# Kernel tuning notes

Measured on AMD Instinct MI355X. Metric: run time of the kernel, lower is better.

## Reference

```python
import jax, jax.numpy as jnp
import numpy as np

N_NODES = 25000
N_EDGES = 400000
FEAT = 128
HID = 64
HEADS = 4
NUM_CLASSES = 2
NUM_GRAPHS = 64


def setup_inputs() -> dict:
    key = jax.random.key(0)
    ks = jax.random.split(key, 16)
    x = jax.random.normal(ks[0], (N_NODES, FEAT), dtype=jnp.float32)
    edge_index = jax.random.randint(ks[1], (2, N_EDGES), 0, N_NODES, dtype=jnp.int32)
    batch = jnp.sort(jax.random.randint(ks[2], (N_NODES,), 0, NUM_GRAPHS, dtype=jnp.int32))
    s = 1.0 / np.sqrt(FEAT)
    sh = 1.0 / np.sqrt(HID)
    shc = 1.0 / np.sqrt(HID * HEADS)
    return {
        "x": x,
        "edge_index": edge_index,
        "batch": batch,
        # conv1: GraphConv(FEAT -> HID): lin_rel (bias) on aggregated neighbors + lin_root (no bias)
        "W1_rel": jax.random.uniform(ks[3], (FEAT, HID), jnp.float32, -s, s),
        "b1": jnp.zeros((HID,), jnp.float32),
        "W1_root": jax.random.uniform(ks[4], (FEAT, HID), jnp.float32, -s, s),
        # conv3: GATConv(HID -> HID, heads=HEADS), concat output [N, HEADS*HID]
        "Wg": jax.random.uniform(ks[5], (HID, HEADS * HID), jnp.float32, -sh, sh),
        "att_src": jax.random.uniform(ks[6], (HEADS, HID), jnp.float32, -sh, sh),
        "att_dst": jax.random.uniform(ks[7], (HEADS, HID), jnp.float32, -sh, sh),
        "bg": jnp.zeros((HEADS * HID,), jnp.float32),
        # conv5: GraphConv(HEADS*HID -> HID)
        "W5_rel": jax.random.uniform(ks[8], (HEADS * HID, HID), jnp.float32, -shc, shc),
        "b5": jnp.zeros((HID,), jnp.float32),
        "W5_root": jax.random.uniform(ks[9], (HEADS * HID, HID), jnp.float32, -shc, shc),
        # fc head
        "W_fc1": jax.random.uniform(ks[10], (HID, HID), jnp.float32, -sh, sh),
        "b_fc1": jnp.zeros((HID,), jnp.float32),
        "W_fc2": jax.random.uniform(ks[11], (HID, NUM_CLASSES), jnp.float32, -sh, sh),
        "b_fc2": jnp.zeros((NUM_CLASSES,), jnp.float32),
    }


def _graph_conv(h, src, dst, W_rel, b, W_root):
    # PyG GraphConv (aggr='add'): out_i = W_rel @ sum_{j->i} h_j + b + W_root @ h_i
    agg = jax.ops.segment_sum(h[src], dst, num_segments=N_NODES)
    return agg @ W_rel + b + h @ W_root


def _gat_conv(h, src, dst, Wg, att_src, att_dst, bg):
    # GATConv with default add_self_loops=True; eval mode (no attn dropout)
    n = h.shape[0]
    loop = jnp.arange(n, dtype=src.dtype)
    si = jnp.concatenate([src, loop])
    di = jnp.concatenate([dst, loop])
    xl = (h @ Wg).reshape(n, HEADS, HID)              # [N, H, C]
    a_s = jnp.sum(xl * att_src, axis=-1)              # [N, H]
    a_d = jnp.sum(xl * att_dst, axis=-1)              # [N, H]
    e = jax.nn.leaky_relu(a_s[si] + a_d[di], 0.2)     # [E', H]
    m = jax.ops.segment_max(e, di, num_segments=n)
    p = jnp.exp(e - m[di])
    denom = jax.ops.segment_sum(p, di, num_segments=n)
    alpha = p / denom[di]                             # segment softmax over incoming edges
    out = jax.ops.segment_sum(alpha[:, :, None] * xl[si], di, num_segments=n)
    return out.reshape(n, HEADS * HID) + bg


def reference(x, edge_index, batch, W1_rel, b1, W1_root, Wg, att_src, att_dst, bg,
              W5_rel, b5, W5_root, W_fc1, b_fc1, W_fc2, b_fc2):
    src, dst = edge_index[0], edge_index[1]
    h = jax.nn.relu(_graph_conv(x, src, dst, W1_rel, b1, W1_root))
    h = jax.nn.relu(_gat_conv(h, src, dst, Wg, att_src, att_dst, bg))
    h = jax.nn.relu(_graph_conv(h, src, dst, W5_rel, b5, W5_root))
    g = jax.ops.segment_sum(h, batch, num_segments=NUM_GRAPHS)   # global_add_pool
    g = jax.nn.relu(g @ W_fc1 + b_fc1)
    return jax.nn.sigmoid(g @ W_fc2 + b_fc2)
```

## Files before the change

kernel.cpp:

```cpp
#include <hip/hip_runtime.h>
#include <math.h>

#define N_NODES 25000
#define N_EDGES 400000
#define FEAT 128
#define HID 64
#define HEADS 4
#define HH 256
#define NUM_GRAPHS 64
#define BUCKET 96
#define HS 1601536
#define NPH 25600

typedef unsigned short ushort_t;
typedef unsigned int uint_t;
typedef __attribute__((ext_vector_type(8))) short short8;
typedef __attribute__((ext_vector_type(4))) float f32x4;

__device__ __forceinline__ float lrelu(float x){ return x > 0.f ? x : 0.2f*x; }

__device__ __forceinline__ ushort_t f2bf(float f){
  uint_t u = __float_as_uint(f);
  return (ushort_t)((u + 0x7fffu + ((u >> 16) & 1u)) >> 16);
}
#define BF_LO(u) __uint_as_float((u) << 16)
#define BF_HI(u) __uint_as_float((u) & 0xffff0000u)

__global__ __launch_bounds__(256) void k_fill(
    const int* __restrict__ src, const int* __restrict__ dst,
    int* __restrict__ cnt, int* __restrict__ slot,
    const float* __restrict__ W1_rel, const float* __restrict__ W1_root,
    const float* __restrict__ W5_rel, const float* __restrict__ W5_root,
    const float* __restrict__ Wg,
    ushort_t* __restrict__ wc1b, ushort_t* __restrict__ wc5b,
    ushort_t* __restrict__ wgb)
{
  const int e = blockIdx.x*256 + threadIdx.x;
  if (blockIdx.x < 64){
    {
      int j=e&7, lane=(e>>3)&63, kc=(e>>9)&3, nt=e>>11;
      int k = kc*32 + (lane>>4)*8 + j, n = nt*16 + (lane&15);
      float v = (n < 64) ? W1_rel[k*64 + n] : W1_root[k*64 + n - 64];
      wc1b[e] = f2bf(v);
    }
    {
      int j=e&7, lane=(e>>3)&63, kt=(e>>9)&1, nt=e>>10;
      int k = kt*32 + (lane>>4)*8 + j, n = nt*16 + (lane&15);
      wgb[e] = f2bf(Wg[k*HH + n]);
    }
    #pragma unroll
    for (int e5 = e; e5 < 32768; e5 += 16384){
      int j=e5&7, lane=(e5>>3)&63, kc=(e5>>9)&7, nt=e5>>12;
      int k = kc*32 + (lane>>4)*8 + j, n = nt*16 + (lane&15);
      float v = (n < 64) ? W5_rel[k*64 + n] : W5_root[k*64 + n - 64];
      wc5b[e5] = f2bf(v);
    }
  }
  if (e < N_EDGES){
    int d = dst[e];
    int pos = atomicAdd(&cnt[d], 1);
    if (pos < BUCKET) slot[(size_t)d*BUCKET + pos] = src[e];
  }
}

__global__ __launch_bounds__(256) void conv1_mfma(
    const float* __restrict__ X, const ushort_t* __restrict__ wc1b,
    const float* __restrict__ bias,
    ushort_t* __restrict__ out_rel_b, float* __restrict__ out_root)
{
  const int wid  = __builtin_amdgcn_readfirstlane(threadIdx.x >> 6);
  const int lane = threadIdx.x & 63;
  const int quad = lane >> 4, col = lane & 15;
  const int nb = blockIdx.x*64 + wid*16;
  if (nb >= N_NODES) return;
  const int row = min(nb + col, N_NODES-1);
  const float* __restrict__ xr = X + (size_t)row*FEAT + quad*8;
  short8 a[4];
  #pragma unroll
  for (int kc = 0; kc < 4; kc++){
    #pragma unroll
    for (int j = 0; j < 8; j++)
      ((ushort_t*)&a[kc])[j] = f2bf(xr[kc*32 + j]);
  }
  #pragma unroll
  for (int nt = 0; nt < 8; nt++){
    f32x4 d = {0.f,0.f,0.f,0.f};
    #pragma unroll
    for (int kc = 0; kc < 4; kc++){
      short8 b = *(const short8*)(wc1b + ((size_t)(nt*4+kc)*64 + lane)*8);
      d = __builtin_amdgcn_mfma_f32_16x16x32_bf16(a[kc], b, d, 0, 0, 0);
    }
    if (nt < 4){
      #pragma unroll
      for (int r = 0; r < 4; r++){
        const int node = nb + quad*4 + r;
        if (node < N_NODES)
          out_rel_b[(size_t)node*HID + nt*16 + col] = f2bf(d[r]);
      }
    } else {
      const float bv = bias[(nt-4)*16 + col];
      #pragma unroll
      for (int r = 0; r < 4; r++){
        const int node = nb + quad*4 + r;
        if (node < N_NODES)
          out_root[(size_t)node*HID + (nt-4)*16 + col] = d[r] + bv;
      }
    }
  }
}

__global__ __launch_bounds__(256) void conv5_mfma(
    const ushort_t* __restrict__ h2b_hm, const ushort_t* __restrict__ wc5b,
    const float* __restrict__ bias,
    ushort_t* __restrict__ out_rel_b, float* __restrict__ out_root)
{
  const int wid  = __builtin_amdgcn_readfirstlane(threadIdx.x >> 6);
  const int lane = threadIdx.x & 63;
  const int quad = lane >> 4, col = lane & 15;
  const int nb = blockIdx.x*64 + wid*16;
  if (nb >= N_NODES) return;
  const int row = nb + col;
  short8 a[8];
  #pragma unroll
  for (int kc = 0; kc < 8; kc++){
    const int k0 = kc*32 + quad*8;
    a[kc] = *(const short8*)(h2b_hm + (size_t)(k0>>6)*HS
                             + (size_t)row*HID + (k0&63));
  }
  #pragma unroll
  for (int nt = 0; nt < 8; nt++){
    f32x4 d = {0.f,0.f,0.f,0.f};
    #pragma unroll
    for (int kc = 0; kc < 8; kc++){
      short8 b = *(const short8*)(wc5b + ((size_t)(nt*8+kc)*64 + lane)*8);
      d = __builtin_amdgcn_mfma_f32_16x16x32_bf16(a[kc], b, d, 0, 0, 0);
    }
    if (nt < 4){
      #pragma unroll
      for (int r = 0; r < 4; r++){
        const int node = nb + quad*4 + r;
        if (node < N_NODES)
          out_rel_b[(size_t)node*HID + nt*16 + col] = f2bf(d[r]);
      }
    } else {
      const float bv = bias[(nt-4)*16 + col];
      #pragma unroll
      for (int r = 0; r < 4; r++){
        const int node = nb + quad*4 + r;
        if (node < N_NODES)
          out_root[(size_t)node*HID + (nt-4)*16 + col] = d[r] + bv;
      }
    }
  }
}

__global__ __launch_bounds__(256) void k3_mfma(
    const ushort_t* __restrict__ h1b, const ushort_t* __restrict__ wgb,
    const float* __restrict__ att_src, const float* __restrict__ att_dst,
    ushort_t* __restrict__ xlb_hm, float* __restrict__ a_s_hm,
    float* __restrict__ a_d_hm)
{
  const int wid  = __builtin_amdgcn_readfirstlane(threadIdx.x >> 6);
  const int lane = threadIdx.x & 63;
  const int quad = lane >> 4, col = lane & 15;
  const int nb = blockIdx.x*64 + wid*16;
  const ushort_t* arow = h1b + (size_t)(nb + col)*HID + quad*8;
  short8 a0 = *(const short8*)(arow);
  short8 a1 = *(const short8*)(arow + 32);
  float as_acc[4] = {0,0,0,0}, ad_acc[4] = {0,0,0,0};
  #pragma unroll
  for (int nt = 0; nt < 16; nt++){
    short8 b0 = *(const short8*)(wgb + ((size_t)(nt*2+0)*64 + lane)*8);
    short8 b1 = *(const short8*)(wgb + ((size_t)(nt*2+1)*64 + lane)*8);
    f32x4 d = {0.f, 0.f, 0.f, 0.f};
    d = __builtin_amdgcn_mfma_f32_16x16x32_bf16(a0, b0, d, 0, 0, 0);
    d = __builtin_amdgcn_mfma_f32_16x16x32_bf16(a1, b1, d, 0, 0, 0);
    const int h = nt >> 2;
    const float asv = att_src[h*HID + (nt & 3)*16 + col];
    const float adv = att_dst[h*HID + (nt & 3)*16 + col];
    #pragma unroll
    for (int r = 0; r < 4; r++){
      const int node = nb + quad*4 + r;
      if (node < N_NODES)
        xlb_hm[(size_t)h*HS + (size_t)node*HID + (nt&3)*16 + col] = f2bf(d[r]);
      as_acc[r] += d[r]*asv;
      ad_acc[r] += d[r]*adv;
    }
    if ((nt & 3) == 3){
      #pragma unroll
      for (int r = 0; r < 4; r++){
        float s1 = as_acc[r], s2 = ad_acc[r];
        #pragma unroll
        for (int off = 1; off < 16; off <<= 1){
          s1 += __shfl_xor(s1, off, 64);
          s2 += __shfl_xor(s2, off, 64);
        }
        const int node = nb + quad*4 + r;
        if (col == 0 && node < N_NODES){
          a_s_hm[h*NPH + node] = s1;
          a_d_hm[h*NPH + node] = s2;
        }
        as_acc[r] = 0.f; ad_acc[r] = 0.f;
      }
    }
  }
}

template<bool BF16OUT>
__global__ __launch_bounds__(256) void k_aggb(
    const int* __restrict__ cnt, const int* __restrict__ slot,
    const ushort_t* __restrict__ featb, const float* __restrict__ root,
    float* __restrict__ outf, ushort_t* __restrict__ outb)
{
  const int node = blockIdx.x*4 + (threadIdx.x >> 6);
  const int lane = threadIdx.x & 63;
  const int* __restrict__ sl = slot + (size_t)node*BUCKET;
  const int deg = min(cnt[node], BUCKET);
  float acc = root[(size_t)node*HID + lane];
  int e = 0;
  for (; e + 4 <= deg; e += 4){
    int sA = sl[e],   sB = sl[e+1];
    int sC = sl[e+2], sD = sl[e+3];
    float xA = BF_LO((uint_t)featb[(size_t)sA*HID + lane]);
    float xB = BF_LO((uint_t)featb[(size_t)sB*HID + lane]);
    float xC = BF_LO((uint_t)featb[(size_t)sC*HID + lane]);
    float xD = BF_LO((uint_t)featb[(size_t)sD*HID + lane]);
    acc += xA; acc += xB; acc += xC; acc += xD;
  }
  for (; e < deg; e++){
    int s = sl[e];
    acc += BF_LO((uint_t)featb[(size_t)s*HID + lane]);
  }
  const float v = fmaxf(acc, 0.f);
  if (BF16OUT) outb[(size_t)node*HID + lane] = f2bf(v);
  else         outf[(size_t)node*HID + lane] = v;
}

__global__ __launch_bounds__(256) void k_gat_node(
    const int* __restrict__ cnt, const int* __restrict__ slot,
    const ushort_t* __restrict__ xlb_hm, const float* __restrict__ a_s_hm,
    const float* __restrict__ a_d_hm, const float* __restrict__ bg,
    ushort_t* __restrict__ h2b_hm)
{
  const int head = blockIdx.x & 3;
  const int node = (blockIdx.x >> 2)*16 + (threadIdx.x >> 4);
  if (node >= N_NODES) return;
  const int lane = threadIdx.x & 63;
  const int cl = lane & 15;
  const int gb = lane & 48;
  const int* __restrict__ sl = slot + (size_t)node*BUCKET;
  const int deg = min(cnt[node], BUCKET);
  const ushort_t* __restrict__ xlh = xlb_hm + (size_t)head*HS;
  const float* __restrict__ ash = a_s_hm + head*NPH;
  const float adh = a_d_hm[head*NPH + node];
  float acc0=0, acc1=0, acc2=0, acc3=0;
  float dsum = 0.f;
  for (int base = 0; base < deg; base += 16){
    float pme = 0.f; int sme = node;
    const int e = base + cl;
    if (e < deg){
      sme = sl[e];
      pme = __expf(lrelu(ash[sme] + adh));
    }
    dsum += pme;
    const int nsub = min(16, deg - base);
    int s = 0;
    for (; s + 2 <= nsub; s += 2){
      const float pA = __shfl(pme, gb + s, 64);
      const int   sA = __shfl(sme, gb + s, 64);
      const float pB = __shfl(pme, gb + s + 1, 64);
      const int   sB = __shfl(sme, gb + s + 1, 64);
      uint2 rA = ((const uint2*)(xlh + (size_t)sA*HID))[cl];
      uint2 rB = ((const uint2*)(xlh + (size_t)sB*HID))[cl];
      acc0 += pA*BF_LO(rA.x); acc1 += pA*BF_HI(rA.x);
      acc2 += pA*BF_LO(rA.y); acc3 += pA*BF_HI(rA.y);
      acc0 += pB*BF_LO(rB.x); acc1 += pB*BF_HI(rB.x);
      acc2 += pB*BF_LO(rB.y); acc3 += pB*BF_HI(rB.y);
    }
    if (s < nsub){
      const float pA = __shfl(pme, gb + s, 64);
      const int   sA = __shfl(sme, gb + s, 64);
      uint2 rA = ((const uint2*)(xlh + (size_t)sA*HID))[cl];
      acc0 += pA*BF_LO(rA.x); acc1 += pA*BF_HI(rA.x);
      acc2 += pA*BF_LO(rA.y); acc3 += pA*BF_HI(rA.y);
    }
  }
  #pragma unroll
  for (int off = 1; off < 16; off <<= 1) dsum += __shfl_xor(dsum, off, 64);
  const float pself = __expf(lrelu(ash[node] + adh));
  const float inv = 1.f / (dsum + pself);
  uint2 r = ((const uint2*)(xlh + (size_t)node*HID))[cl];
  acc0 += pself*BF_LO(r.x); acc1 += pself*BF_HI(r.x);
  acc2 += pself*BF_LO(r.y); acc3 += pself*BF_HI(r.y);
  const int col0 = head*HID + cl*4;
  const float ox = fmaxf(acc0*inv + bg[col0+0], 0.f);
  const float oy = fmaxf(acc1*inv + bg[col0+1], 0.f);
  const float oz = fmaxf(acc2*inv + bg[col0+2], 0.f);
  const float ow = fmaxf(acc3*inv + bg[col0+3], 0.f);
  uint2 o;
  o.x = (uint_t)f2bf(ox) | ((uint_t)f2bf(oy) << 16);
  o.y = (uint_t)f2bf(oz) | ((uint_t)f2bf(ow) << 16);
  ((uint2*)(h2b_hm + (size_t)head*HS + (size_t)node*HID))[cl] = o;
}

__global__ __launch_bounds__(256) void k_pool(
    const float* __restrict__ h3, const int* __restrict__ batch,
    float* __restrict__ g)
{
  const int w = blockIdx.x*4 + (threadIdx.x >> 6);
  const int j = threadIdx.x & 63;
  int n0 = w*64;
  if (n0 >= N_NODES) return;
  int n1 = min(n0+64, N_NODES);
  float acc = 0.f;
  int cur = batch[n0];
  for (int n = n0; n < n1; n++){
    int b = batch[n];
    if (b != cur){ atomicAdd(&g[cur*HID + j], acc); acc = 0.f; cur = b; }
    acc += h3[n*HID + j];
  }
  atomicAdd(&g[cur*HID + j], acc);
}

__global__ __launch_bounds__(256) void k_head(
    const float* __restrict__ g, const float* __restrict__ W1,
    const float* __restrict__ b1, const float* __restrict__ W2,
    const float* __restrict__ b2, float* __restrict__ out)
{
  __shared__ float gs[NUM_GRAPHS*HID];
  __shared__ float hh[NUM_GRAPHS*HID];
  for (int i = threadIdx.x; i < NUM_GRAPHS*HID; i += 256) gs[i] = g[i];
  __syncthreads();
  for (int t = threadIdx.x; t < NUM_GRAPHS*HID; t += 256){
    int b = t >> 6, j = t & 63;
    float acc = b1[j];
    for (int k = 0; k < HID; k++) acc += gs[b*HID+k]*W1[k*HID+j];
    hh[t] = fmaxf(acc, 0.f);
  }
  __syncthreads();
  for (int t = threadIdx.x; t < NUM_GRAPHS*2; t += 256){
    int b = t >> 1, c = t & 1;
    float acc = b2[c];
    for (int k = 0; k < HID; k++) acc += hh[b*HID+k]*W2[k*2+c];
    out[t] = 1.f / (1.f + __expf(-acc));
  }
}

extern "C" void kernel_launch(void* const* d_in, const int* in_sizes, int n_in,
                              void* d_out, int out_size, void* d_ws, size_t ws_size,
                              hipStream_t stream)
{
  const float* x       = (const float*)d_in[0];
  const int*   ei      = (const int*)d_in[1];
  const int*   batch   = (const int*)d_in[2];
  const float* W1_rel  = (const float*)d_in[3];
  const float* b1      = (const float*)d_in[4];
  const float* W1_root = (const float*)d_in[5];
  const float* Wg      = (const float*)d_in[6];
  const float* att_src = (const float*)d_in[7];
  const float* att_dst = (const float*)d_in[8];
  const float* bg      = (const float*)d_in[9];
  const float* W5_rel  = (const float*)d_in[10];
  const float* b5      = (const float*)d_in[11];
  const float* W5_root = (const float*)d_in[12];
  const float* W_fc1   = (const float*)d_in[13];
  const float* b_fc1   = (const float*)d_in[14];
  const float* W_fc2   = (const float*)d_in[15];
  const float* b_fc2   = (const float*)d_in[16];
  const int* src = ei;
  const int* dst = ei + N_EDGES;

  float* ws    = (float*)d_ws;
  ushort_t* xr_b   = (ushort_t*)ws;
  float*    hB     = ws +  800800;
  ushort_t* h1b    = (ushort_t*)(ws + 2402400);
  ushort_t* xlb_hm = (ushort_t*)(ws + 3203200);
  float*    a_s_hm = ws + 6406304;
  float*    a_d_hm = ws + 6508704;
  ushort_t* h2b_hm = (ushort_t*)(ws + 6611104);
  float*    g      = ws + 9814200;
  int*      cnt    = (int*)(ws + 9818296);
  ushort_t* wc1b   = (ushort_t*)(ws + 9843296);
  ushort_t* wc5b   = (ushort_t*)(ws + 9851488);
  ushort_t* wgb    = (ushort_t*)(ws + 9867872);
  int*      slot   = (int*)(ws + 9876064);
  float*    out    = (float*)d_out;

  hipMemsetAsync(g, 0, (4096 + N_NODES)*sizeof(float), stream);
  k_fill<<<(N_EDGES+255)/256,256,0,stream>>>(src, dst, cnt, slot,
      W1_rel, W1_root, W5_rel, W5_root, Wg, wc1b, wc5b, wgb);

  conv1_mfma<<<(N_NODES+63)/64,256,0,stream>>>(x, wc1b, b1, xr_b, hB);
  k_aggb<true><<<N_NODES/4,256,0,stream>>>(cnt, slot, xr_b, hB, nullptr, h1b);

  k3_mfma<<<(N_NODES+63)/64,256,0,stream>>>(h1b, wgb, att_src, att_dst,
                                            xlb_hm, a_s_hm, a_d_hm);
  k_gat_node<<<((N_NODES+15)/16)*HEADS,256,0,stream>>>(cnt, slot,
      xlb_hm, a_s_hm, a_d_hm, bg, h2b_hm);

  conv5_mfma<<<(N_NODES+63)/64,256,0,stream>>>(h2b_hm, wc5b, b5, xr_b, hB);
  k_aggb<false><<<N_NODES/4,256,0,stream>>>(cnt, slot, xr_b, hB, hB, nullptr);

  k_pool<<<(N_NODES/256)+1,256,0,stream>>>(hB, batch, g);
  k_head<<<1,256,0,stream>>>(g, W_fc1, b_fc1, W_fc2, b_fc2, out);
}
```

Measured before the change: 248.2 us.

## Fuse all GNN stages into one cooperative persistent kernel with grid syncs

Replaces the chain of about ten kernel launches and a memset with a single cooperative megakernel. Every stage runs as a grid-stride loop, and stages are separated by grid-wide barriers. The goal is to remove launch overhead and inter-kernel gaps. The cost is that the grid is capped by occupancy, so some stages may get fewer blocks in flight, and each of the roughly ten grid syncs adds its own barrier cost. The original multi-kernel path is kept as a fallback if the cooperative launch fails.

```diff
diff --git a/kernel.cpp b/kernel.cpp
--- a/kernel.cpp
+++ b/kernel.cpp
@@ -1,5 +1,8 @@
 #include <hip/hip_runtime.h>
+#include <hip/hip_cooperative_groups.h>
 #include <math.h>
+
+namespace cg = cooperative_groups;
 
 #define N_NODES 25000
 #define N_EDGES 400000
@@ -18,13 +21,329 @@
 typedef __attribute__((ext_vector_type(4))) float f32x4;
 
 __device__ __forceinline__ float lrelu(float x){ return x > 0.f ? x : 0.2f*x; }
-
 __device__ __forceinline__ ushort_t f2bf(float f){
   uint_t u = __float_as_uint(f);
   return (ushort_t)((u + 0x7fffu + ((u >> 16) & 1u)) >> 16);
 }
 #define BF_LO(u) __uint_as_float((u) << 16)
 #define BF_HI(u) __uint_as_float((u) & 0xffff0000u)
+
+__global__ __launch_bounds__(256) void mega(
+    const float* __restrict__ x, const int* __restrict__ srcp,
+    const int* __restrict__ dstp, const int* __restrict__ batch,
+    const float* __restrict__ W1_rel, const float* __restrict__ b1,
+    const float* __restrict__ W1_root, const float* __restrict__ Wg,
+    const float* __restrict__ att_src, const float* __restrict__ att_dst,
+    const float* __restrict__ bg, const float* __restrict__ W5_rel,
+    const float* __restrict__ b5, const float* __restrict__ W5_root,
+    const float* __restrict__ W_fc1, const float* __restrict__ b_fc1,
+    const float* __restrict__ W_fc2, const float* __restrict__ b_fc2,
+    ushort_t* __restrict__ xr_b, float* __restrict__ hB,
+    ushort_t* __restrict__ h1b, ushort_t* __restrict__ xlb_hm,
+    float* __restrict__ a_s_hm, float* __restrict__ a_d_hm,
+    ushort_t* __restrict__ h2b_hm, float* __restrict__ g, int* __restrict__ cnt,
+    ushort_t* __restrict__ wc1b, ushort_t* __restrict__ wc5b,
+    ushort_t* __restrict__ wgb, int* __restrict__ slot, float* __restrict__ out)
+{
+  __shared__ float gs[NUM_GRAPHS*HID];
+  __shared__ float hh[NUM_GRAPHS*HID];
+  const int tid = threadIdx.x;
+  const int NB = gridDim.x;
+  const int NT = NB*256;
+  const int gtid = blockIdx.x*256 + tid;
+  const int wid  = tid >> 6;
+  const int lane = tid & 63;
+  const int quad = lane >> 4, col = lane & 15;
+
+  for (int i = gtid; i < 4096 + 25024; i += NT){
+    if (i < 4096) g[i] = 0.f; else cnt[i-4096] = 0;
+  }
+  cg::this_grid().sync();
+
+  for (int e = gtid; e < 16384; e += NT){
+    { int j=e&7, l=(e>>3)&63, kc=(e>>9)&3, nt=e>>11;
+      int k = kc*32 + (l>>4)*8 + j, n = nt*16 + (l&15);
+      float v = (n < 64) ? W1_rel[k*64 + n] : W1_root[k*64 + n - 64];
+      wc1b[e] = f2bf(v); }
+    { int j=e&7, l=(e>>3)&63, kt=(e>>9)&1, nt=e>>10;
+      int k = kt*32 + (l>>4)*8 + j, n = nt*16 + (l&15);
+      wgb[e] = f2bf(Wg[k*HH + n]); }
+  }
+  for (int e = gtid; e < 32768; e += NT){
+    int j=e&7, l=(e>>3)&63, kc=(e>>9)&7, nt=e>>12;
+    int k = kc*32 + (l>>4)*8 + j, n = nt*16 + (l&15);
+    float v = (n < 64) ? W5_rel[k*64 + n] : W5_root[k*64 + n - 64];
+    wc5b[e] = f2bf(v);
+  }
+  for (int e = gtid; e < N_EDGES; e += NT){
+    int d = dstp[e];
+    int pos = atomicAdd(&cnt[d], 1);
+    if (pos < BUCKET) slot[(size_t)d*BUCKET + pos] = srcp[e];
+  }
+  cg::this_grid().sync();
+
+  for (int tile = blockIdx.x; tile < 391; tile += NB){
+    const int nb = tile*64 + wid*16;
+    if (nb < N_NODES){
+      const int row = min(nb + col, N_NODES-1);
+      const float* xr = x + (size_t)row*FEAT + quad*8;
+      short8 a[4];
+      #pragma unroll
+      for (int kc = 0; kc < 4; kc++){
+        #pragma unroll
+        for (int j = 0; j < 8; j++)
+          ((ushort_t*)&a[kc])[j] = f2bf(xr[kc*32 + j]);
+      }
+      #pragma unroll
+      for (int nt = 0; nt < 8; nt++){
+        f32x4 d = {0.f,0.f,0.f,0.f};
+        #pragma unroll
+        for (int kc = 0; kc < 4; kc++){
+          short8 b = *(const short8*)(wc1b + ((size_t)(nt*4+kc)*64 + lane)*8);
+          d = __builtin_amdgcn_mfma_f32_16x16x32_bf16(a[kc], b, d, 0, 0, 0);
+        }
+        if (nt < 4){
+          #pragma unroll
+          for (int r = 0; r < 4; r++){
+            const int node = nb + quad*4 + r;
+            if (node < N_NODES)
+              xr_b[(size_t)node*HID + nt*16 + col] = f2bf(d[r]);
+          }
+        } else {
+          const float bv = b1[(nt-4)*16 + col];
+          #pragma unroll
+          for (int r = 0; r < 4; r++){
+            const int node = nb + quad*4 + r;
+            if (node < N_NODES)
+              hB[(size_t)node*HID + (nt-4)*16 + col] = d[r] + bv;
+          }
+        }
+      }
+    }
+  }
+  cg::this_grid().sync();
+
+  for (int grp = blockIdx.x; grp < 6250; grp += NB){
+    const int node = grp*4 + wid;
+    const int* sl = slot + (size_t)node*BUCKET;
+    const int deg = min(cnt[node], BUCKET);
+    float acc = hB[(size_t)node*HID + lane];
+    int e = 0;
+    for (; e + 4 <= deg; e += 4){
+      int sA = sl[e], sB = sl[e+1], sC = sl[e+2], sD = sl[e+3];
+      acc += BF_LO((uint_t)xr_b[(size_t)sA*HID + lane]);
+      acc += BF_LO((uint_t)xr_b[(size_t)sB*HID + lane]);
+      acc += BF_LO((uint_t)xr_b[(size_t)sC*HID + lane]);
+      acc += BF_LO((uint_t)xr_b[(size_t)sD*HID + lane]);
+    }
+    for (; e < deg; e++)
+      acc += BF_LO((uint_t)xr_b[(size_t)sl[e]*HID + lane]);
+    h1b[(size_t)node*HID + lane] = f2bf(fmaxf(acc, 0.f));
+  }
+  cg::this_grid().sync();
+
+  for (int tile = blockIdx.x; tile < 391; tile += NB){
+    const int nb = tile*64 + wid*16;
+    const ushort_t* arow = h1b + (size_t)(nb + col)*HID + quad*8;
+    short8 a0 = *(const short8*)(arow);
+    short8 a1 = *(const short8*)(arow + 32);
+    float as_acc[4] = {0,0,0,0}, ad_acc[4] = {0,0,0,0};
+    #pragma unroll
+    for (int nt = 0; nt < 16; nt++){
+      short8 b0 = *(const short8*)(wgb + ((size_t)(nt*2+0)*64 + lane)*8);
+      short8 b1v = *(const short8*)(wgb + ((size_t)(nt*2+1)*64 + lane)*8);
+      f32x4 d = {0.f, 0.f, 0.f, 0.f};
+      d = __builtin_amdgcn_mfma_f32_16x16x32_bf16(a0, b0, d, 0, 0, 0);
+      d = __builtin_amdgcn_mfma_f32_16x16x32_bf16(a1, b1v, d, 0, 0, 0);
+      const int h = nt >> 2;
+      const float asv = att_src[h*HID + (nt & 3)*16 + col];
+      const float adv = att_dst[h*HID + (nt & 3)*16 + col];
+      #pragma unroll
+      for (int r = 0; r < 4; r++){
+        const int node = nb + quad*4 + r;
+        if (node < N_NODES)
+          xlb_hm[(size_t)h*HS + (size_t)node*HID + (nt&3)*16 + col] = f2bf(d[r]);
+        as_acc[r] += d[r]*asv;
+        ad_acc[r] += d[r]*adv;
+      }
+      if ((nt & 3) == 3){
+        #pragma unroll
+        for (int r = 0; r < 4; r++){
+          float s1 = as_acc[r], s2 = ad_acc[r];
+          #pragma unroll
+          for (int off = 1; off < 16; off <<= 1){
+            s1 += __shfl_xor(s1, off, 64);
+            s2 += __shfl_xor(s2, off, 64);
+          }
+          const int node = nb + quad*4 + r;
+          if (col == 0 && node < N_NODES){
+            a_s_hm[h*NPH + node] = s1;
+            a_d_hm[h*NPH + node] = s2;
+          }
+          as_acc[r] = 0.f; ad_acc[r] = 0.f;
+        }
+      }
+    }
+  }
+  cg::this_grid().sync();
+
+  for (int vb = blockIdx.x; vb < 6252; vb += NB){
+    const int head = vb & 3;
+    const int node = (vb >> 2)*16 + (tid >> 4);
+    if (node < N_NODES){
+      const int cl = lane & 15;
+      const int gb = lane & 48;
+      const int* sl = slot + (size_t)node*BUCKET;
+      const int deg = min(cnt[node], BUCKET);
+      const ushort_t* xlh = xlb_hm + (size_t)head*HS;
+      const float* ash = a_s_hm + head*NPH;
+      const float adh = a_d_hm[head*NPH + node];
+      float acc0=0, acc1=0, acc2=0, acc3=0;
+      float dsum = 0.f;
+      for (int base = 0; base < deg; base += 16){
+        float pme = 0.f; int sme = node;
+        const int e = base + cl;
+        if (e < deg){
+          sme = sl[e];
+          pme = __expf(lrelu(ash[sme] + adh));
+        }
+        dsum += pme;
+        const int nsub = min(16, deg - base);
+        int s = 0;
+        for (; s + 2 <= nsub; s += 2){
+          const float pA = __shfl(pme, gb + s, 64);
+          const int   sA = __shfl(sme, gb + s, 64);
+          const float pB = __shfl(pme, gb + s + 1, 64);
+          const int   sB = __shfl(sme, gb + s + 1, 64);
+          uint2 rA = ((const uint2*)(xlh + (size_t)sA*HID))[cl];
+          uint2 rB = ((const uint2*)(xlh + (size_t)sB*HID))[cl];
+          acc0 += pA*BF_LO(rA.x); acc1 += pA*BF_HI(rA.x);
+          acc2 += pA*BF_LO(rA.y); acc3 += pA*BF_HI(rA.y);
+          acc0 += pB*BF_LO(rB.x); acc1 += pB*BF_HI(rB.x);
+          acc2 += pB*BF_LO(rB.y); acc3 += pB*BF_HI(rB.y);
+        }
+        if (s < nsub){
+          const float pA = __shfl(pme, gb + s, 64);
+          const int   sA = __shfl(sme, gb + s, 64);
+          uint2 rA = ((const uint2*)(xlh + (size_t)sA*HID))[cl];
+          acc0 += pA*BF_LO(rA.x); acc1 += pA*BF_HI(rA.x);
+          acc2 += pA*BF_LO(rA.y); acc3 += pA*BF_HI(rA.y);
+        }
+      }
+      #pragma unroll
+      for (int off = 1; off < 16; off <<= 1) dsum += __shfl_xor(dsum, off, 64);
+      const float pself = __expf(lrelu(ash[node] + adh));
+      const float inv = 1.f / (dsum + pself);
+      uint2 r = ((const uint2*)(xlh + (size_t)node*HID))[cl];
+      acc0 += pself*BF_LO(r.x); acc1 += pself*BF_HI(r.x);
+      acc2 += pself*BF_LO(r.y); acc3 += pself*BF_HI(r.y);
+      const int col0 = head*HID + cl*4;
+      const float ox = fmaxf(acc0*inv + bg[col0+0], 0.f);
+      const float oy = fmaxf(acc1*inv + bg[col0+1], 0.f);
+      const float oz = fmaxf(acc2*inv + bg[col0+2], 0.f);
+      const float ow = fmaxf(acc3*inv + bg[col0+3], 0.f);
+      uint2 o;
+      o.x = (uint_t)f2bf(ox) | ((uint_t)f2bf(oy) << 16);
+      o.y = (uint_t)f2bf(oz) | ((uint_t)f2bf(ow) << 16);
+      ((uint2*)(h2b_hm + (size_t)head*HS + (size_t)node*HID))[cl] = o;
+    }
+  }
+  cg::this_grid().sync();
+
+  for (int tile = blockIdx.x; tile < 391; tile += NB){
+    const int nb = tile*64 + wid*16;
+    if (nb < N_NODES){
+      const int row = nb + col;
+      short8 a[8];
+      #pragma unroll
+      for (int kc = 0; kc < 8; kc++){
+        const int k0 = kc*32 + quad*8;
+        a[kc] = *(const short8*)(h2b_hm + (size_t)(k0>>6)*HS
+                                 + (size_t)row*HID + (k0&63));
+      }
+      #pragma unroll
+      for (int nt = 0; nt < 8; nt++){
+        f32x4 d = {0.f,0.f,0.f,0.f};
+        #pragma unroll
+        for (int kc = 0; kc < 8; kc++){
+          short8 b = *(const short8*)(wc5b + ((size_t)(nt*8+kc)*64 + lane)*8);
+          d = __builtin_amdgcn_mfma_f32_16x16x32_bf16(a[kc], b, d, 0, 0, 0);
+        }
+        if (nt < 4){
+          #pragma unroll
+          for (int r = 0; r < 4; r++){
+            const int node = nb + quad*4 + r;
+            if (node < N_NODES)
+              xr_b[(size_t)node*HID + nt*16 + col] = f2bf(d[r]);
+          }
+        } else {
+          const float bv = b5[(nt-4)*16 + col];
+          #pragma unroll
+          for (int r = 0; r < 4; r++){
+            const int node = nb + quad*4 + r;
+            if (node < N_NODES)
+              hB[(size_t)node*HID + (nt-4)*16 + col] = d[r] + bv;
+          }
+        }
+      }
+    }
+  }
+  cg::this_grid().sync();
+
+  for (int grp = blockIdx.x; grp < 6250; grp += NB){
+    const int node = grp*4 + wid;
+    const int* sl = slot + (size_t)node*BUCKET;
+    const int deg = min(cnt[node], BUCKET);
+    float acc = hB[(size_t)node*HID + lane];
+    int e = 0;
+    for (; e + 4 <= deg; e += 4){
+      int sA = sl[e], sB = sl[e+1], sC = sl[e+2], sD = sl[e+3];
+      acc += BF_LO((uint_t)xr_b[(size_t)sA*HID + lane]);
+      acc += BF_LO((uint_t)xr_b[(size_t)sB*HID + lane]);
+      acc += BF_LO((uint_t)xr_b[(size_t)sC*HID + lane]);
+      acc += BF_LO((uint_t)xr_b[(size_t)sD*HID + lane]);
+    }
+    for (; e < deg; e++)
+      acc += BF_LO((uint_t)xr_b[(size_t)sl[e]*HID + lane]);
+    hB[(size_t)node*HID + lane] = fmaxf(acc, 0.f);
+  }
+  cg::this_grid().sync();
+
+  for (int vb = blockIdx.x; vb < 98; vb += NB){
+    const int w = vb*4 + wid;
+    const int n0 = w*64;
+    if (n0 < N_NODES){
+      const int n1 = min(n0+64, N_NODES);
+      float acc = 0.f;
+      int cur = batch[n0];
+      for (int n = n0; n < n1; n++){
+        int b = batch[n];
+        if (b != cur){ atomicAdd(&g[cur*HID + lane], acc); acc = 0.f; cur = b; }
+        acc += hB[(size_t)n*HID + lane];
+      }
+      atomicAdd(&g[cur*HID + lane], acc);
+    }
+  }
+  cg::this_grid().sync();
+
+  if (blockIdx.x == 0){
+    for (int i = tid; i < NUM_GRAPHS*HID; i += 256) gs[i] = g[i];
+    __syncthreads();
+    for (int t = tid; t < NUM_GRAPHS*HID; t += 256){
+      int b = t >> 6, j = t & 63;
+      float acc = b_fc1[j];
+      for (int k = 0; k < HID; k++) acc += gs[b*HID+k]*W_fc1[k*HID+j];
+      hh[t] = fmaxf(acc, 0.f);
+    }
+    __syncthreads();
+    for (int t = tid; t < NUM_GRAPHS*2; t += 256){
+      int b = t >> 1, c = t & 1;
+      float acc = b_fc2[c];
+      for (int k = 0; k < HID; k++) acc += hh[b*HID+k]*W_fc2[k*2+c];
+      out[t] = 1.f / (1.f + __expf(-acc));
+    }
+  }
+}
 
 __global__ __launch_bounds__(256) void k_fill(
     const int* __restrict__ src, const int* __restrict__ dst,
@@ -37,17 +356,13 @@
 {
   const int e = blockIdx.x*256 + threadIdx.x;
   if (blockIdx.x < 64){
-    {
-      int j=e&7, lane=(e>>3)&63, kc=(e>>9)&3, nt=e>>11;
+    { int j=e&7, lane=(e>>3)&63, kc=(e>>9)&3, nt=e>>11;
       int k = kc*32 + (lane>>4)*8 + j, n = nt*16 + (lane&15);
       float v = (n < 64) ? W1_rel[k*64 + n] : W1_root[k*64 + n - 64];
-      wc1b[e] = f2bf(v);
-    }
-    {
-      int j=e&7, lane=(e>>3)&63, kt=(e>>9)&1, nt=e>>10;
+      wc1b[e] = f2bf(v); }
+    { int j=e&7, lane=(e>>3)&63, kt=(e>>9)&1, nt=e>>10;
       int k = kt*32 + (lane>>4)*8 + j, n = nt*16 + (lane&15);
-      wgb[e] = f2bf(Wg[k*HH + n]);
-    }
+      wgb[e] = f2bf(Wg[k*HH + n]); }
     #pragma unroll
     for (int e5 = e; e5 < 32768; e5 += 16384){
       int j=e5&7, lane=(e5>>3)&63, kc=(e5>>9)&7, nt=e5>>12;
@@ -221,16 +536,13 @@
   for (; e + 4 <= deg; e += 4){
     int sA = sl[e],   sB = sl[e+1];
     int sC = sl[e+2], sD = sl[e+3];
-    float xA = BF_LO((uint_t)featb[(size_t)sA*HID + lane]);
-    float xB = BF_LO((uint_t)featb[(size_t)sB*HID + lane]);
-    float xC = BF_LO((uint_t)featb[(size_t)sC*HID + lane]);
-    float xD = BF_LO((uint_t)featb[(size_t)sD*HID + lane]);
-    acc += xA; acc += xB; acc += xC; acc += xD;
-  }
-  for (; e < deg; e++){
-    int s = sl[e];
-    acc += BF_LO((uint_t)featb[(size_t)s*HID + lane]);
-  }
+    acc += BF_LO((uint_t)featb[(size_t)sA*HID + lane]);
+    acc += BF_LO((uint_t)featb[(size_t)sB*HID + lane]);
+    acc += BF_LO((uint_t)featb[(size_t)sC*HID + lane]);
+    acc += BF_LO((uint_t)featb[(size_t)sD*HID + lane]);
+  }
+  for (; e < deg; e++)
+    acc += BF_LO((uint_t)featb[(size_t)sl[e]*HID + lane]);
   const float v = fmaxf(acc, 0.f);
   if (BF16OUT) outb[(size_t)node*HID + lane] = f2bf(v);
   else         outf[(size_t)node*HID + lane] = v;
@@ -380,27 +692,46 @@
   ushort_t* h2b_hm = (ushort_t*)(ws + 6611104);
   float*    g      = ws + 9814200;
   int*      cnt    = (int*)(ws + 9818296);
-  ushort_t* wc1b   = (ushort_t*)(ws + 9843296);
-  ushort_t* wc5b   = (ushort_t*)(ws + 9851488);
-  ushort_t* wgb    = (ushort_t*)(ws + 9867872);
-  int*      slot   = (int*)(ws + 9876064);
+  ushort_t* wc1b   = (ushort_t*)(ws + 9843320);
+  ushort_t* wc5b   = (ushort_t*)(ws + 9851512);
+  ushort_t* wgb    = (ushort_t*)(ws + 9867896);
+  int*      slot   = (int*)(ws + 9876088);
   float*    out    = (float*)d_out;
 
-  hipMemsetAsync(g, 0, (4096 + N_NODES)*sizeof(float), stream);
+  int occ = 0;
+  hipError_t oe = hipOccupancyMaxActiveBlocksPerMultiprocessor(
+      &occ, (const void*)mega, 256, 0);
+  int NB = (oe == hipSuccess && occ > 0) ? occ*256 : 0;
+  if (NB > 1563) NB = 1563;
+  bool coop_done = false;
+  if (NB >= 256){
+    void* args[] = {
+      (void*)&x, (void*)&src, (void*)&dst, (void*)&batch,
+      (void*)&W1_rel, (void*)&b1, (void*)&W1_root, (void*)&Wg,
+      (void*)&att_src, (void*)&att_dst, (void*)&bg, (void*)&W5_rel,
+      (void*)&b5, (void*)&W5_root, (void*)&W_fc1, (void*)&b_fc1,
+      (void*)&W_fc2, (void*)&b_fc2,
+      (void*)&xr_b, (void*)&hB, (void*)&h1b, (void*)&xlb_hm,
+      (void*)&a_s_hm, (void*)&a_d_hm, (void*)&h2b_hm, (void*)&g, (void*)&cnt,
+      (void*)&wc1b, (void*)&wc5b, (void*)&wgb, (void*)&slot, (void*)&out
+    };
+    hipError_t err = hipLaunchCooperativeKernel(
+        (const void*)mega, dim3(NB), dim3(256), args, 0, stream);
+    coop_done = (err == hipSuccess);
+  }
+  if (coop_done) return;
+
+  hipMemsetAsync(g, 0, (4096 + 25024)*sizeof(float), stream);
   k_fill<<<(N_EDGES+255)/256,256,0,stream>>>(src, dst, cnt, slot,
       W1_rel, W1_root, W5_rel, W5_root, Wg, wc1b, wc5b, wgb);
-
   conv1_mfma<<<(N_NODES+63)/64,256,0,stream>>>(x, wc1b, b1, xr_b, hB);
   k_aggb<true><<<N_NODES/4,256,0,stream>>>(cnt, slot, xr_b, hB, nullptr, h1b);
-
   k3_mfma<<<(N_NODES+63)/64,256,0,stream>>>(h1b, wgb, att_src, att_dst,
                                             xlb_hm, a_s_hm, a_d_hm);
   k_gat_node<<<((N_NODES+15)/16)*HEADS,256,0,stream>>>(cnt, slot,
       xlb_hm, a_s_hm, a_d_hm, bg, h2b_hm);
-
   conv5_mfma<<<(N_NODES+63)/64,256,0,stream>>>(h2b_hm, wc5b, b5, xr_b, hB);
   k_aggb<false><<<N_NODES/4,256,0,stream>>>(cnt, slot, xr_b, hB, hB, nullptr);
-
   k_pool<<<(N_NODES/256)+1,256,0,stream>>>(hB, batch, g);
   k_head<<<1,256,0,stream>>>(g, W_fc1, b_fc1, W_fc2, b_fc2, out);
 }
```

Result: slower. 730.8 us (+194.4%).
